# Optimization experiments

Measured on AMD Instinct MI355X. Metric: run time of the kernel, lower is better.

The kernel has to match this reference:

```python
import jax, jax.numpy as jnp
import numpy as np

S, B, C = 7, 2, 20
LAMBDA_COORD = 5.0
LAMBDA_NOOBJ = 0.5
WH_EPS = 1e-6
IOU_EPS = 1e-6
BATCH = 16384


def _iou_yolo(a, b):
    # a, b: [..., 4] in (cx, cy, w, h) 'yolo' center format
    ax1, ay1 = a[..., 0] - a[..., 2] / 2, a[..., 1] - a[..., 3] / 2
    ax2, ay2 = a[..., 0] + a[..., 2] / 2, a[..., 1] + a[..., 3] / 2
    bx1, by1 = b[..., 0] - b[..., 2] / 2, b[..., 1] - b[..., 3] / 2
    bx2, by2 = b[..., 0] + b[..., 2] / 2, b[..., 1] + b[..., 3] / 2
    iw = jnp.clip(jnp.minimum(ax2, bx2) - jnp.maximum(ax1, bx1), 0.0)
    ih = jnp.clip(jnp.minimum(ay2, by2) - jnp.maximum(ay1, by1), 0.0)
    inter = iw * ih
    area_a = jnp.abs((ax2 - ax1) * (ay2 - ay1))
    area_b = jnp.abs((bx2 - bx1) * (by2 - by1))
    return inter / (area_a + area_b - inter + IOU_EPS)


def setup_inputs() -> dict:
    key = jax.random.key(0)
    k1, k2, k3 = jax.random.split(key, 3)
    D = C + 5 * B  # 30
    y_trues = jax.random.uniform(k1, (BATCH, S, S, D), dtype=jnp.float32)
    # conf channel must be exactly 0.0 or 1.0 (loss branches on == 1)
    conf = (jax.random.uniform(k2, (BATCH, S, S)) < 0.3).astype(jnp.float32)
    y_trues = y_trues.at[..., 4].set(conf)
    y_preds = jax.random.normal(k3, (BATCH, S, S, D), dtype=jnp.float32)
    return {"y_trues": y_trues, "y_preds": y_preds}


def reference(y_trues, y_preds):
    D = C + 5 * B
    t = y_trues.reshape(-1, S * S, D)   # [N, 49, 30]
    p = y_preds.reshape(-1, S * S, D)
    batch_size = p.shape[0]

    b = t[..., 0:4]
    bhat1 = p[..., 0:4]
    bhat2 = p[..., 5:9]

    iou1 = _iou_yolo(b, bhat1)          # [N, 49]
    iou2 = _iou_yolo(b, bhat2)
    use1 = iou1 > iou2

    bhat = jnp.where(use1[..., None], bhat1, bhat2)            # responsible box
    confhat_chosen = jnp.where(use1, p[..., 4], p[..., 9])
    confhat_other = jnp.where(use1, p[..., 9], p[..., 4])

    # coord losses (object cells)
    xy = LAMBDA_COORD * ((b[..., 0] - bhat[..., 0]) ** 2 + (b[..., 1] - bhat[..., 1]) ** 2)
    wh = LAMBDA_COORD * (
        (jnp.sqrt(b[..., 2]) - jnp.sqrt(jnp.abs(bhat[..., 2] + WH_EPS))) ** 2
        + (jnp.sqrt(b[..., 3]) - jnp.sqrt(jnp.abs(bhat[..., 3] + WH_EPS))) ** 2
    )
    obj_conf = (t[..., 4] - confhat_chosen) ** 2
    noobj_in_obj = LAMBDA_NOOBJ * (0.0 - confhat_other) ** 2
    cls = jnp.sum((t[..., 10:] - p[..., 10:]) ** 2, axis=-1)

    obj_terms = xy + wh + obj_conf + noobj_in_obj + cls

    # no-object cells: penalize both predicted confs toward y_true conf (== target conf channel)
    noobj_terms = LAMBDA_NOOBJ * (
        (t[..., 4] - p[..., 4]) ** 2 + (t[..., 4] - p[..., 9]) ** 2
    )

    obj_mask = t[..., 4] == 1.0
    total = jnp.sum(jnp.where(obj_mask, obj_terms, noobj_terms))
    return total / batch_size
```

## Files before the change

kernel.cpp:

```cpp
#include <hip/hip_runtime.h>

#define LAMBDA_COORD 5.0f
#define LAMBDA_NOOBJ 0.5f
#define WH_EPS 1e-6f
#define IOU_EPS 1e-6f

__device__ __forceinline__ float iou_yolo(float a0, float a1, float a2, float a3,
                                          float b0, float b1, float b2, float b3) {
    float ax1 = a0 - a2 * 0.5f, ay1 = a1 - a3 * 0.5f;
    float ax2 = a0 + a2 * 0.5f, ay2 = a1 + a3 * 0.5f;
    float bx1 = b0 - b2 * 0.5f, by1 = b1 - b3 * 0.5f;
    float bx2 = b0 + b2 * 0.5f, by2 = b1 + b3 * 0.5f;
    float iw = fmaxf(fminf(ax2, bx2) - fmaxf(ax1, bx1), 0.0f);
    float ih = fmaxf(fminf(ay2, by2) - fmaxf(ay1, by1), 0.0f);
    float inter = iw * ih;
    float area_a = fabsf((ax2 - ax1) * (ay2 - ay1));
    float area_b = fabsf((bx2 - bx1) * (by2 - by1));
    return inter / (area_a + area_b - inter + IOU_EPS);
}

__global__ __launch_bounds__(256, 4) void yolo_loss_kernel(
    const float* __restrict__ t_g, const float* __restrict__ p_g,
    float* __restrict__ out, int n_cells, float inv_batch) {
    const int c = blockIdx.x * blockDim.x + threadIdx.x;

    float v = 0.0f;
    if (c < n_cells) {
        const float2* tv = (const float2*)t_g + (size_t)c * 15;
        const float2* pv = (const float2*)p_g + (size_t)c * 15;

        float2 T[15], P[15];
#pragma unroll
        for (int i = 0; i < 15; ++i) T[i] = tv[i];
#pragma unroll
        for (int i = 0; i < 15; ++i) P[i] = pv[i];

        const float b0 = T[0].x, b1 = T[0].y, b2 = T[1].x, b3 = T[1].y, t4 = T[2].x;
        const float p0 = P[0].x, p1 = P[0].y, p2 = P[1].x, p3 = P[1].y, p4 = P[2].x;
        const float p5 = P[2].y, p6 = P[3].x, p7 = P[3].y, p8 = P[4].x, p9 = P[4].y;

        float iou1 = iou_yolo(b0, b1, b2, b3, p0, p1, p2, p3);
        float iou2 = iou_yolo(b0, b1, b2, b3, p5, p6, p7, p8);
        bool use1 = iou1 > iou2;

        float bh0 = use1 ? p0 : p5;
        float bh1 = use1 ? p1 : p6;
        float bh2 = use1 ? p2 : p7;
        float bh3 = use1 ? p3 : p8;
        float conf_c = use1 ? p4 : p9;
        float conf_o = use1 ? p9 : p4;

        float dx = b0 - bh0, dy = b1 - bh1;
        float xy = LAMBDA_COORD * (dx * dx + dy * dy);

        float sw = sqrtf(b2) - sqrtf(fabsf(bh2 + WH_EPS));
        float sh = sqrtf(b3) - sqrtf(fabsf(bh3 + WH_EPS));
        float wh = LAMBDA_COORD * (sw * sw + sh * sh);

        float dc = t4 - conf_c;
        float obj_conf = dc * dc;
        float noobj_in_obj = LAMBDA_NOOBJ * conf_o * conf_o;

        float cls = 0.0f;
#pragma unroll
        for (int i = 5; i < 15; ++i) {
            float dxc = T[i].x - P[i].x;
            float dyc = T[i].y - P[i].y;
            cls += dxc * dxc + dyc * dyc;
        }

        float obj_terms = xy + wh + obj_conf + noobj_in_obj + cls;

        float d4 = t4 - p4, d9 = t4 - p9;
        float noobj_terms = LAMBDA_NOOBJ * (d4 * d4 + d9 * d9);

        v = (t4 == 1.0f) ? obj_terms : noobj_terms;
    }

#pragma unroll
    for (int off = 32; off > 0; off >>= 1)
        v += __shfl_down(v, off, 64);

    __shared__ float swave[4];
    const int lane = threadIdx.x & 63;
    const int wid = threadIdx.x >> 6;
    if (lane == 0) swave[wid] = v;
    __syncthreads();
    if (threadIdx.x == 0) {
        float s = swave[0] + swave[1] + swave[2] + swave[3];
        atomicAdd(out, s * inv_batch);
    }
}

extern "C" void kernel_launch(void* const* d_in, const int* in_sizes, int n_in,
                              void* d_out, int out_size, void* d_ws, size_t ws_size,
                              hipStream_t stream) {
    const float* t = (const float*)d_in[0];
    const float* p = (const float*)d_in[1];
    float* out = (float*)d_out;

    const int total = in_sizes[0];
    const int cells = total / 30;
    const int batch = cells / 49;
    const float inv_batch = 1.0f / (float)batch;

    hipMemsetAsync(out, 0, sizeof(float), stream);

    const int block = 256;
    const int grid = (cells + block - 1) / block;
    yolo_loss_kernel<<<grid, block, 0, stream>>>(t, p, out, cells, inv_batch);
}
```

Measured before the change: 214.0 us.

## Load cells cooperatively per wave with coalesced float4 and shuffle-based box gathering

Each wave now processes groups of 8 cells (240 floats) with 60 lanes each loading one float4 from each input, so global loads are fully coalesced. The old layout had every thread read its own strided 120-byte cell. Class-term squared differences are computed in place with a per-lane mask. The box and confidence fields for the two cells in each 15-lane segment are gathered with cross-lane shuffles. The launch also switches to a fixed grid-stride grid of 1792 blocks, which adds shuffle overhead and redundant per-lane cell computation. It also assumes the cell count is a multiple of 8, which holds here (16384*49 cells).

```diff
diff --git a/kernel.cpp b/kernel.cpp
--- a/kernel.cpp
+++ b/kernel.cpp
@@ -4,6 +4,8 @@
 #define LAMBDA_NOOBJ 0.5f
 #define WH_EPS 1e-6f
 #define IOU_EPS 1e-6f
+
+constexpr int BLOCKS = 1792;
 
 __device__ __forceinline__ float iou_yolo(float a0, float a1, float a2, float a3,
                                           float b0, float b1, float b2, float b3) {
@@ -19,62 +21,107 @@
     return inter / (area_a + area_b - inter + IOU_EPS);
 }
 
-__global__ __launch_bounds__(256, 4) void yolo_loss_kernel(
-    const float* __restrict__ t_g, const float* __restrict__ p_g,
-    float* __restrict__ out, int n_cells, float inv_batch) {
-    const int c = blockIdx.x * blockDim.x + threadIdx.x;
+__device__ __forceinline__ float cell_terms(
+    float b0, float b1, float b2, float b3, float t4,
+    float p0, float p1, float p2, float p3, float p4,
+    float p5, float p6, float p7, float p8, float p9) {
+    float iou1 = iou_yolo(b0, b1, b2, b3, p0, p1, p2, p3);
+    float iou2 = iou_yolo(b0, b1, b2, b3, p5, p6, p7, p8);
+    bool use1 = iou1 > iou2;
+
+    float bh0 = use1 ? p0 : p5;
+    float bh1 = use1 ? p1 : p6;
+    float bh2 = use1 ? p2 : p7;
+    float bh3 = use1 ? p3 : p8;
+    float conf_c = use1 ? p4 : p9;
+    float conf_o = use1 ? p9 : p4;
+
+    float dx = b0 - bh0, dy = b1 - bh1;
+    float xy = LAMBDA_COORD * (dx * dx + dy * dy);
+
+    float sw = sqrtf(b2) - sqrtf(fabsf(bh2 + WH_EPS));
+    float sh = sqrtf(b3) - sqrtf(fabsf(bh3 + WH_EPS));
+    float wh = LAMBDA_COORD * (sw * sw + sh * sh);
+
+    float dc = t4 - conf_c;
+    float obj_terms = xy + wh + dc * dc + LAMBDA_NOOBJ * conf_o * conf_o;
+
+    float d4 = t4 - p4, d9 = t4 - p9;
+    float noobj_terms = LAMBDA_NOOBJ * (d4 * d4 + d9 * d9);
+
+    return (t4 == 1.0f) ? obj_terms : noobj_terms;
+}
+
+__global__ __launch_bounds__(256) void yolo_loss_kernel(
+    const float4* __restrict__ tv, const float4* __restrict__ pv,
+    float* __restrict__ out, int ngroups, float inv_batch) {
+    const int lane = threadIdx.x & 63;
+    const int widx = threadIdx.x >> 6;
+    const int wave_id = blockIdx.x * 4 + widx;
+    const int nwaves = gridDim.x * 4;
+
+    const int u = lane % 15;
+    const int bbase = lane - u;
+    const bool active = lane < 60;
+
+    float cm[4];
+#pragma unroll
+    for (int j = 0; j < 4; ++j) {
+        int idx = 4 * u + j;
+        bool isA = (idx >= 10 && idx < 30);
+        bool isB = (idx >= 40);
+        cm[j] = (isA || isB) ? 1.0f : 0.0f;
+    }
+    const bool sideA = (u <= 7);
 
     float v = 0.0f;
-    if (c < n_cells) {
-        const float2* tv = (const float2*)t_g + (size_t)c * 15;
-        const float2* pv = (const float2*)p_g + (size_t)c * 15;
 
-        float2 T[15], P[15];
-#pragma unroll
-        for (int i = 0; i < 15; ++i) T[i] = tv[i];
-#pragma unroll
-        for (int i = 0; i < 15; ++i) P[i] = pv[i];
-
-        const float b0 = T[0].x, b1 = T[0].y, b2 = T[1].x, b3 = T[1].y, t4 = T[2].x;
-        const float p0 = P[0].x, p1 = P[0].y, p2 = P[1].x, p3 = P[1].y, p4 = P[2].x;
-        const float p5 = P[2].y, p6 = P[3].x, p7 = P[3].y, p8 = P[4].x, p9 = P[4].y;
-
-        float iou1 = iou_yolo(b0, b1, b2, b3, p0, p1, p2, p3);
-        float iou2 = iou_yolo(b0, b1, b2, b3, p5, p6, p7, p8);
-        bool use1 = iou1 > iou2;
-
-        float bh0 = use1 ? p0 : p5;
-        float bh1 = use1 ? p1 : p6;
-        float bh2 = use1 ? p2 : p7;
-        float bh3 = use1 ? p3 : p8;
-        float conf_c = use1 ? p4 : p9;
-        float conf_o = use1 ? p9 : p4;
-
-        float dx = b0 - bh0, dy = b1 - bh1;
-        float xy = LAMBDA_COORD * (dx * dx + dy * dy);
-
-        float sw = sqrtf(b2) - sqrtf(fabsf(bh2 + WH_EPS));
-        float sh = sqrtf(b3) - sqrtf(fabsf(bh3 + WH_EPS));
-        float wh = LAMBDA_COORD * (sw * sw + sh * sh);
-
-        float dc = t4 - conf_c;
-        float obj_conf = dc * dc;
-        float noobj_in_obj = LAMBDA_NOOBJ * conf_o * conf_o;
-
-        float cls = 0.0f;
-#pragma unroll
-        for (int i = 5; i < 15; ++i) {
-            float dxc = T[i].x - P[i].x;
-            float dyc = T[i].y - P[i].y;
-            cls += dxc * dxc + dyc * dyc;
+    for (int g = wave_id; g < ngroups; g += nwaves) {
+        float4 T = make_float4(0.f, 0.f, 0.f, 0.f);
+        float4 P = make_float4(0.f, 0.f, 0.f, 0.f);
+        if (active) {
+            size_t base = (size_t)g * 60 + lane;
+            T = tv[base];
+            P = pv[base];
         }
 
-        float obj_terms = xy + wh + obj_conf + noobj_in_obj + cls;
+        float d0 = T.x - P.x, d1 = T.y - P.y, d2 = T.z - P.z, d3 = T.w - P.w;
+        float s_cls = d0 * d0 * cm[0] + d1 * d1 * cm[1] +
+                      d2 * d2 * cm[2] + d3 * d3 * cm[3];
 
-        float d4 = t4 - p4, d9 = t4 - p9;
-        float noobj_terms = LAMBDA_NOOBJ * (d4 * d4 + d9 * d9);
+        float t4A = __shfl(T.x, bbase + 1, 64);
+        float t4B = __shfl(T.z, bbase + 8, 64);
+        float objm = ((sideA ? t4A : t4B) == 1.0f) ? 1.0f : 0.0f;
+        v += s_cls * objm;
 
-        v = (t4 == 1.0f) ? obj_terms : noobj_terms;
+        float a_b0 = __shfl(T.x, bbase, 64);
+        float a_b1 = __shfl(T.y, bbase, 64);
+        float a_b2 = __shfl(T.z, bbase, 64);
+        float a_b3 = __shfl(T.w, bbase, 64);
+        float a_p0 = __shfl(P.x, bbase, 64);
+        float a_p1 = __shfl(P.y, bbase, 64);
+        float a_p2 = __shfl(P.z, bbase, 64);
+        float a_p3 = __shfl(P.w, bbase, 64);
+        float a_p8 = __shfl(P.x, bbase + 2, 64);
+        float a_p9 = __shfl(P.y, bbase + 2, 64);
+
+        float b_b0 = __shfl(T.z, bbase + 7, 64);
+        float b_b1 = __shfl(T.w, bbase + 7, 64);
+        float b_p0 = __shfl(P.z, bbase + 7, 64);
+        float b_p1 = __shfl(P.w, bbase + 7, 64);
+        float b_p6 = __shfl(P.x, bbase + 9, 64);
+        float b_p7 = __shfl(P.y, bbase + 9, 64);
+        float b_p8 = __shfl(P.z, bbase + 9, 64);
+        float b_p9 = __shfl(P.w, bbase + 9, 64);
+
+        float cA = cell_terms(a_b0, a_b1, a_b2, a_b3, T.x,
+                              a_p0, a_p1, a_p2, a_p3, P.x,
+                              P.y, P.z, P.w, a_p8, a_p9);
+        float cB = cell_terms(b_b0, b_b1, T.x, T.y, T.z,
+                              b_p0, b_p1, P.x, P.y, P.z,
+                              P.w, b_p6, b_p7, b_p8, b_p9);
+        if (active && u == 1) v += cA;
+        if (active && u == 8) v += cB;
     }
 
 #pragma unroll
@@ -82,9 +129,7 @@
         v += __shfl_down(v, off, 64);
 
     __shared__ float swave[4];
-    const int lane = threadIdx.x & 63;
-    const int wid = threadIdx.x >> 6;
-    if (lane == 0) swave[wid] = v;
+    if ((threadIdx.x & 63) == 0) swave[widx] = v;
     __syncthreads();
     if (threadIdx.x == 0) {
         float s = swave[0] + swave[1] + swave[2] + swave[3];
@@ -101,12 +146,12 @@
 
     const int total = in_sizes[0];
     const int cells = total / 30;
+    const int ngroups = cells / 8;
     const int batch = cells / 49;
     const float inv_batch = 1.0f / (float)batch;
 
     hipMemsetAsync(out, 0, sizeof(float), stream);
 
-    const int block = 256;
-    const int grid = (cells + block - 1) / block;
-    yolo_loss_kernel<<<grid, block, 0, stream>>>(t, p, out, cells, inv_batch);
+    yolo_loss_kernel<<<BLOCKS, 256, 0, stream>>>(
+        (const float4*)t, (const float4*)p, out, ngroups, inv_batch);
 }
```

Measured after the change: 212.9 us. About the same (-0.5%).
